# Optimization experiments

Measured on AMD Instinct MI355X. Metric: run time of the kernel, lower is better.

Reference implementation:

```python
import jax, jax.numpy as jnp
import numpy as np

NUM_HEADS = 6

def setup_inputs() -> dict:
    key = jax.random.key(0)
    k1, k2, k3, k4 = jax.random.split(key, 4)
    B, T, C = 128, 256, 384
    s = 1.0 / np.sqrt(C)
    return {
        'x': jax.random.normal(k1, (B, T, C), dtype=jnp.float32),
        'Wq': jax.random.normal(k2, (C, C), dtype=jnp.float32) * s,
        'Wk': jax.random.normal(k3, (C, C), dtype=jnp.float32) * s,
        'Wv': jax.random.normal(k4, (C, C), dtype=jnp.float32) * s,
    }

def reference(x, Wq, Wk, Wv):
    B, T, C = x.shape
    H = NUM_HEADS
    d = C // H
    # projections (bias-free Linear), split into heads
    q = (x @ Wq).reshape(B, T, H, d)
    k = (x @ Wk).reshape(B, T, H, d)
    v = (x @ Wv).reshape(B, T, H, d)
    # NOTE: original scales by 1/sqrt(C), not 1/sqrt(head_dim)
    scale = 1.0 / jnp.sqrt(jnp.asarray(C, dtype=x.dtype))
    att = jnp.einsum('bqhd,bkhd->bhqk', q, k) * scale  # [B,H,T,T]
    causal = jnp.tril(jnp.ones((T, T), dtype=bool))
    att = jnp.where(causal, att, -jnp.inf)
    att = jax.nn.softmax(att, axis=-1)
    # dropout is identity in eval/deterministic mode
    out = jnp.einsum('bhqk,bkhd->bqhd', att, v)  # [B,T,H,d]
    return out.reshape(B, T, C)
```

## Files before the change

kernel.cpp:

```cpp
#include <hip/hip_runtime.h>


typedef unsigned short u16;
typedef float f32x4 __attribute__((ext_vector_type(4)));
typedef short s16x8 __attribute__((ext_vector_type(8)));
typedef u16 u16x4 __attribute__((ext_vector_type(4)));

static constexpr int BB = 128;
static constexpr int TT = 256;
static constexpr int CC = 384;
static constexpr int HH = 6;
static constexpr int DD = 64;
static constexpr int MM = BB * TT;

static constexpr size_t WTOFF = 0;
static constexpr size_t XOFF  = (size_t)3 * CC * CC;

static constexpr float CSC = 0.07362242194579907f;

__device__ __forceinline__ u16 f2bf(float f) {
  unsigned u = __float_as_uint(f);
  u += 0x7fffu + ((u >> 16) & 1u);
  return (u16)(u >> 16);
}

__device__ __forceinline__ void g2l16(const u16* g, u16* l) {
  __builtin_amdgcn_global_load_lds(
      (const __attribute__((address_space(1))) u16*)g,
      (__attribute__((address_space(3))) u16*)l, 16, 0, 0);
}

__global__ void prep(const float* __restrict__ X, const float* __restrict__ Wq,
                     const float* __restrict__ Wk, const float* __restrict__ Wv,
                     u16* __restrict__ ws) {
  int bx = blockIdx.x;
  if (bx < 6144) {
    size_t i = (size_t)(bx * 256 + threadIdx.x) * 8;
    f32x4 a0 = *(const f32x4*)(X + i);
    f32x4 a1 = *(const f32x4*)(X + i + 4);
    s16x8 ab;
#pragma unroll
    for (int j = 0; j < 4; ++j) { ab[j] = (short)f2bf(a0[j]); ab[4 + j] = (short)f2bf(a1[j]); }
    *(s16x8*)(ws + XOFF + i) = ab;
  } else {
    __shared__ u16 Lt[64][66];
    int j = bx - 6144;
    int z = j / 36, t = j % 36, ti = t / 6, tj = t % 6;
    const float* W = (z == 0) ? Wq : (z == 1) ? Wk : Wv;
    const float sc = (z == 0) ? CSC : 1.0f;
    u16* WT = ws + WTOFF + (size_t)z * CC * CC;
    const int rl = threadIdx.x >> 4;
    const int cl = (threadIdx.x & 15) * 4;
#pragma unroll
    for (int it = 0; it < 4; ++it) {
      int r = it * 16 + rl;
      f32x4 v = *(const f32x4*)(W + (size_t)(ti * 64 + r) * CC + tj * 64 + cl);
#pragma unroll
      for (int q = 0; q < 4; ++q) Lt[r][cl + q] = f2bf(v[q] * sc);
    }
    __syncthreads();
#pragma unroll
    for (int it = 0; it < 4; ++it) {
      int n = it * 16 + rl;
      u16x4 o;
#pragma unroll
      for (int q = 0; q < 4; ++q) o[q] = Lt[cl + q][n];
      *(u16x4*)(WT + (size_t)(tj * 64 + n) * CC + ti * 64 + cl) = o;
    }
  }
}

__global__ __launch_bounds__(512, 2) void fused(const u16* __restrict__ ws,
                                                float* __restrict__ out) {
  const int bid = blockIdx.x;
  const int xc = bid & 7;
  const int g5 = bid >> 3;
  const int b = xc * 16 + g5 / 6;
  const int h = g5 % 6;

  __shared__ u16 R1[256][64];
  __shared__ u16 R2[16384];
  __shared__ u16 Ks[256][64];
  __shared__ u16 VTs[64][256];

  const int tid = threadIdx.x;
  const int lane = tid & 63;
  const int w = tid >> 6;
  const int quad = lane >> 4;
  const int col = lane & 15;

  const u16* Xg = ws + XOFF + (size_t)b * TT * CC;
  const u16* Wg = ws + WTOFF;
  u16* Wst = R2;

  const int rl = lane >> 3;
  const int gb = (lane & 7) ^ rl;

  const int wm = (w >> 1) * 64;
  const int wn = (w & 1) * 96;

  auto stage = [&](int kt) {
#pragma unroll
    for (int i = 0; i < 4; ++i) {
      int r0 = w * 32 + i * 8;
      g2l16(Xg + (size_t)(r0 + rl) * CC + kt * 64 + gb * 8, &R1[r0][0]);
    }
#pragma unroll
    for (int i = 0; i < 3; ++i) {
      int r0 = w * 24 + i * 8;
      int rr = r0 + rl;
      int z = rr >> 6, nn = rr & 63;
      g2l16(Wg + (size_t)(z * CC + h * DD + nn) * CC + kt * 64 + gb * 8,
            Wst + r0 * 64);
    }
  };

  f32x4 acc[4][6] = {};

  stage(0);
  __syncthreads();

  for (int kt = 0; kt < 6; ++kt) {
    s16x8 af[4][2], bf[6][2];
#pragma unroll
    for (int mt = 0; mt < 4; ++mt)
#pragma unroll
      for (int ks = 0; ks < 2; ++ks)
        af[mt][ks] = *(const s16x8*)(&R1[wm + mt * 16 + col]
                                        [(((ks * 4 + quad) ^ (col & 7)) * 8)]);
#pragma unroll
    for (int nt = 0; nt < 6; ++nt)
#pragma unroll
      for (int ks = 0; ks < 2; ++ks)
        bf[nt][ks] = *(const s16x8*)(Wst + (wn + nt * 16 + col) * 64 +
                                     (((ks * 4 + quad) ^ (col & 7)) * 8));

    __syncthreads();
    if (kt < 5) stage(kt + 1);

    __builtin_amdgcn_s_setprio(1);
#pragma unroll
    for (int ks = 0; ks < 2; ++ks)
#pragma unroll
      for (int mt = 0; mt < 4; ++mt)
#pragma unroll
        for (int nt = 0; nt < 6; ++nt)
          acc[mt][nt] = __builtin_amdgcn_mfma_f32_16x16x32_bf16(
              af[mt][ks], bf[nt][ks], acc[mt][nt], 0, 0, 0);
    __builtin_amdgcn_s_setprio(0);

    if (kt < 5) __syncthreads();
  }

#pragma unroll
  for (int mt = 0; mt < 4; ++mt) {
    int tokb = wm + mt * 16 + quad * 4;
#pragma unroll
    for (int nt = 0; nt < 6; ++nt) {
      int gn = wn + nt * 16 + col;
      if (gn < 128) {
        u16* dst = (gn < 64) ? &R1[0][0] : &Ks[0][0];
        int d = gn & 63;
#pragma unroll
        for (int r = 0; r < 4; ++r) {
          int tok = tokb + r;
          dst[tok * 64 + (d ^ ((tok & 7) << 3))] = f2bf(acc[mt][nt][r]);
        }
      } else {
        int d = gn - 128;
        uint2 pk;
        pk.x = (unsigned)f2bf(acc[mt][nt][0]) | ((unsigned)f2bf(acc[mt][nt][1]) << 16);
        pk.y = (unsigned)f2bf(acc[mt][nt][2]) | ((unsigned)f2bf(acc[mt][nt][3]) << 16);
        *(uint2*)((u16*)VTs + d * 256 + (tokb ^ ((d & 15) << 3))) = pk;
      }
    }
  }
  __syncthreads();

  const int g0 = w, g1 = 15 - w;
  const int k0max = g0 >> 2, k1max = g1 >> 2;
  const int qq0 = (g0 & 3) * 16 + col;
  const int qq1 = (g1 & 3) * 16 + col;
  u16* PsA = R2 + w * 2048;
  u16* PsB = PsA + 1024;

  s16x8 qf[2][2];
  {
    int qr0 = g0 * 16 + col, qr1 = g1 * 16 + col;
#pragma unroll
    for (int ks = 0; ks < 2; ++ks) {
      qf[0][ks] = *(const s16x8*)(&R1[qr0][(((ks * 4 + quad) ^ (col & 7)) * 8)]);
      qf[1][ks] = *(const s16x8*)(&R1[qr1][(((ks * 4 + quad) ^ (col & 7)) * 8)]);
    }
  }

  f32x4 o[2][4] = {};
  float mst[2] = {-1.0e30f, -1.0e30f}, lst[2] = {0.0f, 0.0f};

  auto sm = [&](f32x4 (&s)[4], bool diag, int qq, float& m, float& l,
                unsigned (&pk)[4][2]) -> float {
    float rmax = -1.0e30f;
#pragma unroll
    for (int nt = 0; nt < 4; ++nt)
#pragma unroll
      for (int r = 0; r < 4; ++r) {
        float t = s[nt][r];
        if (diag && (nt * 16 + quad * 4 + r) > qq) t = -1.0e30f;
        s[nt][r] = t;
        rmax = fmaxf(rmax, t);
      }
    rmax = fmaxf(rmax, __shfl_xor(rmax, 16));
    rmax = fmaxf(rmax, __shfl_xor(rmax, 32));
    float mn = fmaxf(m, rmax);
    float alpha = exp2f(m - mn);
    m = mn;
    float lsum = 0.0f;
#pragma unroll
    for (int nt = 0; nt < 4; ++nt) {
      float p0 = exp2f(s[nt][0] - mn), p1 = exp2f(s[nt][1] - mn);
      float p2 = exp2f(s[nt][2] - mn), p3 = exp2f(s[nt][3] - mn);
      lsum += (p0 + p1) + (p2 + p3);
      pk[nt][0] = (unsigned)f2bf(p0) | ((unsigned)f2bf(p1) << 16);
      pk[nt][1] = (unsigned)f2bf(p2) | ((unsigned)f2bf(p3) << 16);
    }
    l = l * alpha + lsum;
    return alpha;
  };

  for (int kt = 0; kt <= k1max; ++kt) {
    const bool both = (kt <= k0max);

    s16x8 kf[4][2], vf[4][2];
#pragma unroll
    for (int nt = 0; nt < 4; ++nt)
#pragma unroll
      for (int ks = 0; ks < 2; ++ks) {
        int key = kt * 64 + nt * 16 + col;
        kf[nt][ks] = *(const s16x8*)(&Ks[key][(((ks * 4 + quad) ^ (col & 7)) * 8)]);
        int d = nt * 16 + col;
        vf[nt][ks] = *(const s16x8*)((const u16*)VTs + d * 256 +
                     ((kt * 64 + ks * 32 + quad * 8) ^ ((d & 15) << 3)));
      }

    f32x4 sA[4] = {}, sB[4] = {};
    __builtin_amdgcn_s_setprio(1);
    if (both) {
#pragma unroll
      for (int ks = 0; ks < 2; ++ks)
#pragma unroll
        for (int nt = 0; nt < 4; ++nt)
          sA[nt] = __builtin_amdgcn_mfma_f32_16x16x32_bf16(kf[nt][ks], qf[0][ks],
                                                           sA[nt], 0, 0, 0);
    }
#pragma unroll
    for (int ks = 0; ks < 2; ++ks)
#pragma unroll
      for (int nt = 0; nt < 4; ++nt)
        sB[nt] = __builtin_amdgcn_mfma_f32_16x16x32_bf16(kf[nt][ks], qf[1][ks],
                                                         sB[nt], 0, 0, 0);
    __builtin_amdgcn_s_setprio(0);

    unsigned pkA[4][2], pkB[4][2];
    float aA = 1.0f, aB;
    if (both) {
      aA = sm(sA, kt == k0max, qq0, mst[0], lst[0], pkA);
#pragma unroll
      for (int nt = 0; nt < 4; ++nt)
        *(uint2*)(PsA + col * 64 + ((nt * 16 + quad * 4) ^ ((col & 7) << 3))) =
            make_uint2(pkA[nt][0], pkA[nt][1]);
    }
    aB = sm(sB, kt == k1max, qq1, mst[1], lst[1], pkB);
#pragma unroll
    for (int nt = 0; nt < 4; ++nt)
      *(uint2*)(PsB + col * 64 + ((nt * 16 + quad * 4) ^ ((col & 7) << 3))) =
          make_uint2(pkB[nt][0], pkB[nt][1]);

    if (both) {
#pragma unroll
      for (int dt = 0; dt < 4; ++dt)
#pragma unroll
        for (int r = 0; r < 4; ++r) o[0][dt][r] *= aA;
    }
#pragma unroll
    for (int dt = 0; dt < 4; ++dt)
#pragma unroll
      for (int r = 0; r < 4; ++r) o[1][dt][r] *= aB;

    asm volatile("s_waitcnt lgkmcnt(0)" ::: "memory");

    s16x8 pfA[2], pfB[2];
    if (both) {
#pragma unroll
      for (int ks = 0; ks < 2; ++ks)
        pfA[ks] = *(const s16x8*)(PsA + col * 64 +
                                  ((ks * 32 + quad * 8) ^ ((col & 7) << 3)));
    }
#pragma unroll
    for (int ks = 0; ks < 2; ++ks)
      pfB[ks] = *(const s16x8*)(PsB + col * 64 +
                                ((ks * 32 + quad * 8) ^ ((col & 7) << 3)));

    __builtin_amdgcn_s_setprio(1);
    if (both) {
#pragma unroll
      for (int ks = 0; ks < 2; ++ks)
#pragma unroll
        for (int dt = 0; dt < 4; ++dt)
          o[0][dt] = __builtin_amdgcn_mfma_f32_16x16x32_bf16(vf[dt][ks], pfA[ks],
                                                             o[0][dt], 0, 0, 0);
    }
#pragma unroll
    for (int ks = 0; ks < 2; ++ks)
#pragma unroll
      for (int dt = 0; dt < 4; ++dt)
        o[1][dt] = __builtin_amdgcn_mfma_f32_16x16x32_bf16(vf[dt][ks], pfB[ks],
                                                           o[1][dt], 0, 0, 0);
    __builtin_amdgcn_s_setprio(0);
  }

#pragma unroll
  for (int gi = 0; gi < 2; ++gi) {
    int g = gi ? g1 : g0;
    float l = lst[gi];
    l += __shfl_xor(l, 16);
    l += __shfl_xor(l, 32);
    float inv = 1.0f / l;
    int q = g * 16 + col;
#pragma unroll
    for (int dt = 0; dt < 4; ++dt) {
      f32x4 res;
#pragma unroll
      for (int r = 0; r < 4; ++r) res[r] = o[gi][dt][r] * inv;
      *(f32x4*)(out + (size_t)(b * TT + q) * CC + h * DD + dt * 16 + quad * 4) = res;
    }
  }
}

extern "C" void kernel_launch(void* const* d_in, const int* in_sizes, int n_in,
                              void* d_out, int out_size, void* d_ws, size_t ws_size,
                              hipStream_t stream) {
  const float* x  = (const float*)d_in[0];
  const float* wq = (const float*)d_in[1];
  const float* wk = (const float*)d_in[2];
  const float* wv = (const float*)d_in[3];
  u16* ws  = (u16*)d_ws;
  float* out = (float*)d_out;

  prep<<<dim3(6144 + 108), 256, 0, stream>>>(x, wq, wk, wv, ws);
  fused<<<dim3(BB * HH), 512, 0, stream>>>(ws, out);
}
```

Baseline: 154.9 us.

## Double-buffer projection staging, use packed bf16 convert, defer softmax rescale

The QKV projection loop now uses two X and W LDS buffers and prefetches two k-steps ahead. It waits with explicit vmcnt counts and a barrier instead of two __syncthreads per step, aiming to overlap global-to-LDS loads with MFMA work. Float-to-bf16 conversion switches from manual rounding to the hardware v_cvt_pk_bf16_f32 instruction. The online softmax skips the running-max update and output rescale when the new max exceeds the old one by at most 8 across the wave, trading a bounded growth of un-normalised values for fewer exp and multiply ops. The reuse of LDS regions changes: Q and K now live in the X buffers and P in the W buffers.

```diff
diff --git a/kernel.cpp b/kernel.cpp
--- a/kernel.cpp
+++ b/kernel.cpp
@@ -22,6 +22,12 @@
   unsigned u = __float_as_uint(f);
   u += 0x7fffu + ((u >> 16) & 1u);
   return (u16)(u >> 16);
+}
+
+__device__ __forceinline__ unsigned cvtpk(float lo, float hi) {
+  unsigned r;
+  asm("v_cvt_pk_bf16_f32 %0, %1, %2" : "=v"(r) : "v"(lo), "v"(hi));
+  return r;
 }
 
 __device__ __forceinline__ void g2l16(const u16* g, u16* l) {
@@ -78,9 +84,8 @@
   const int b = xc * 16 + g5 / 6;
   const int h = g5 % 6;
 
-  __shared__ u16 R1[256][64];
-  __shared__ u16 R2[16384];
-  __shared__ u16 Ks[256][64];
+  __shared__ u16 X2[2][256][64];
+  __shared__ u16 W2[2][192][64];
   __shared__ u16 VTs[64][256];
 
   const int tid = threadIdx.x;
@@ -91,7 +96,6 @@
 
   const u16* Xg = ws + XOFF + (size_t)b * TT * CC;
   const u16* Wg = ws + WTOFF;
-  u16* Wst = R2;
 
   const int rl = lane >> 3;
   const int gb = (lane & 7) ^ rl;
@@ -100,10 +104,11 @@
   const int wn = (w & 1) * 96;
 
   auto stage = [&](int kt) {
+    int bufi = kt & 1;
 #pragma unroll
     for (int i = 0; i < 4; ++i) {
       int r0 = w * 32 + i * 8;
-      g2l16(Xg + (size_t)(r0 + rl) * CC + kt * 64 + gb * 8, &R1[r0][0]);
+      g2l16(Xg + (size_t)(r0 + rl) * CC + kt * 64 + gb * 8, &X2[bufi][r0][0]);
     }
 #pragma unroll
     for (int i = 0; i < 3; ++i) {
@@ -111,32 +116,42 @@
       int rr = r0 + rl;
       int z = rr >> 6, nn = rr & 63;
       g2l16(Wg + (size_t)(z * CC + h * DD + nn) * CC + kt * 64 + gb * 8,
-            Wst + r0 * 64);
+            &W2[bufi][r0][0]);
     }
   };
 
   f32x4 acc[4][6] = {};
 
   stage(0);
-  __syncthreads();
+  stage(1);
 
   for (int kt = 0; kt < 6; ++kt) {
+    if (kt < 5) asm volatile("s_waitcnt vmcnt(7)" ::: "memory");
+    else        asm volatile("s_waitcnt vmcnt(0)" ::: "memory");
+    __builtin_amdgcn_s_barrier();
+    __builtin_amdgcn_sched_barrier(0);
+
+    const int bufi = kt & 1;
     s16x8 af[4][2], bf[6][2];
 #pragma unroll
     for (int mt = 0; mt < 4; ++mt)
 #pragma unroll
       for (int ks = 0; ks < 2; ++ks)
-        af[mt][ks] = *(const s16x8*)(&R1[wm + mt * 16 + col]
+        af[mt][ks] = *(const s16x8*)(&X2[bufi][wm + mt * 16 + col]
                                         [(((ks * 4 + quad) ^ (col & 7)) * 8)]);
 #pragma unroll
     for (int nt = 0; nt < 6; ++nt)
 #pragma unroll
       for (int ks = 0; ks < 2; ++ks)
-        bf[nt][ks] = *(const s16x8*)(Wst + (wn + nt * 16 + col) * 64 +
-                                     (((ks * 4 + quad) ^ (col & 7)) * 8));
-
-    __syncthreads();
-    if (kt < 5) stage(kt + 1);
+        bf[nt][ks] = *(const s16x8*)(&W2[bufi][wn + nt * 16 + col]
+                                        [(((ks * 4 + quad) ^ (col & 7)) * 8)]);
+
+    if (kt < 4) {
+      asm volatile("s_waitcnt lgkmcnt(0)" ::: "memory");
+      __builtin_amdgcn_s_barrier();
+      __builtin_amdgcn_sched_barrier(0);
+      stage(kt + 2);
+    }
 
     __builtin_amdgcn_s_setprio(1);
 #pragma unroll
@@ -148,30 +163,31 @@
           acc[mt][nt] = __builtin_amdgcn_mfma_f32_16x16x32_bf16(
               af[mt][ks], bf[nt][ks], acc[mt][nt], 0, 0, 0);
     __builtin_amdgcn_s_setprio(0);
-
-    if (kt < 5) __syncthreads();
-  }
-
+  }
+
+  __syncthreads();
+
+  u16* Qb  = &X2[0][0][0];
+  u16* KsB = &X2[1][0][0];
 #pragma unroll
   for (int mt = 0; mt < 4; ++mt) {
     int tokb = wm + mt * 16 + quad * 4;
 #pragma unroll
     for (int nt = 0; nt < 6; ++nt) {
       int gn = wn + nt * 16 + col;
+      unsigned u01 = cvtpk(acc[mt][nt][0], acc[mt][nt][1]);
+      unsigned u23 = cvtpk(acc[mt][nt][2], acc[mt][nt][3]);
       if (gn < 128) {
-        u16* dst = (gn < 64) ? &R1[0][0] : &Ks[0][0];
+        u16* dst = (gn < 64) ? Qb : KsB;
         int d = gn & 63;
-#pragma unroll
-        for (int r = 0; r < 4; ++r) {
-          int tok = tokb + r;
-          dst[tok * 64 + (d ^ ((tok & 7) << 3))] = f2bf(acc[mt][nt][r]);
-        }
+        dst[(tokb + 0) * 64 + (d ^ (((tokb + 0) & 7) << 3))] = (u16)u01;
+        dst[(tokb + 1) * 64 + (d ^ (((tokb + 1) & 7) << 3))] = (u16)(u01 >> 16);
+        dst[(tokb + 2) * 64 + (d ^ (((tokb + 2) & 7) << 3))] = (u16)u23;
+        dst[(tokb + 3) * 64 + (d ^ (((tokb + 3) & 7) << 3))] = (u16)(u23 >> 16);
       } else {
         int d = gn - 128;
-        uint2 pk;
-        pk.x = (unsigned)f2bf(acc[mt][nt][0]) | ((unsigned)f2bf(acc[mt][nt][1]) << 16);
-        pk.y = (unsigned)f2bf(acc[mt][nt][2]) | ((unsigned)f2bf(acc[mt][nt][3]) << 16);
-        *(uint2*)((u16*)VTs + d * 256 + (tokb ^ ((d & 15) << 3))) = pk;
+        *(uint2*)((u16*)VTs + d * 256 + (tokb ^ ((d & 15) << 3))) =
+            make_uint2(u01, u23);
       }
     }
   }
@@ -181,7 +197,7 @@
   const int k0max = g0 >> 2, k1max = g1 >> 2;
   const int qq0 = (g0 & 3) * 16 + col;
   const int qq1 = (g1 & 3) * 16 + col;
-  u16* PsA = R2 + w * 2048;
+  u16* PsA = (u16*)W2 + w * 2048;
   u16* PsB = PsA + 1024;
 
   s16x8 qf[2][2];
@@ -189,8 +205,8 @@
     int qr0 = g0 * 16 + col, qr1 = g1 * 16 + col;
 #pragma unroll
     for (int ks = 0; ks < 2; ++ks) {
-      qf[0][ks] = *(const s16x8*)(&R1[qr0][(((ks * 4 + quad) ^ (col & 7)) * 8)]);
-      qf[1][ks] = *(const s16x8*)(&R1[qr1][(((ks * 4 + quad) ^ (col & 7)) * 8)]);
+      qf[0][ks] = *(const s16x8*)(Qb + qr0 * 64 + (((ks * 4 + quad) ^ (col & 7)) * 8));
+      qf[1][ks] = *(const s16x8*)(Qb + qr1 * 64 + (((ks * 4 + quad) ^ (col & 7)) * 8));
     }
   }
 
@@ -198,30 +214,36 @@
   float mst[2] = {-1.0e30f, -1.0e30f}, lst[2] = {0.0f, 0.0f};
 
   auto sm = [&](f32x4 (&s)[4], bool diag, int qq, float& m, float& l,
-                unsigned (&pk)[4][2]) -> float {
-    float rmax = -1.0e30f;
-#pragma unroll
-    for (int nt = 0; nt < 4; ++nt)
-#pragma unroll
-      for (int r = 0; r < 4; ++r) {
-        float t = s[nt][r];
-        if (diag && (nt * 16 + quad * 4 + r) > qq) t = -1.0e30f;
-        s[nt][r] = t;
-        rmax = fmaxf(rmax, t);
+                unsigned (&pk)[4][2], bool& deferred) -> float {
+    float mx[4];
+#pragma unroll
+    for (int nt = 0; nt < 4; ++nt) {
+      if (diag) {
+#pragma unroll
+        for (int r = 0; r < 4; ++r)
+          if ((nt * 16 + quad * 4 + r) > qq) s[nt][r] = -1.0e30f;
       }
+      mx[nt] = fmaxf(fmaxf(s[nt][0], s[nt][1]), fmaxf(s[nt][2], s[nt][3]));
+    }
+    float rmax = fmaxf(fmaxf(mx[0], mx[1]), fmaxf(mx[2], mx[3]));
     rmax = fmaxf(rmax, __shfl_xor(rmax, 16));
     rmax = fmaxf(rmax, __shfl_xor(rmax, 32));
-    float mn = fmaxf(m, rmax);
-    float alpha = exp2f(m - mn);
-    m = mn;
+
+    deferred = __all(rmax - m <= 8.0f);
+    float alpha = 1.0f;
+    if (!deferred) {
+      float mn = fmaxf(m, rmax);
+      alpha = exp2f(m - mn);
+      m = mn;
+    }
     float lsum = 0.0f;
 #pragma unroll
     for (int nt = 0; nt < 4; ++nt) {
-      float p0 = exp2f(s[nt][0] - mn), p1 = exp2f(s[nt][1] - mn);
-      float p2 = exp2f(s[nt][2] - mn), p3 = exp2f(s[nt][3] - mn);
+      float p0 = exp2f(s[nt][0] - m), p1 = exp2f(s[nt][1] - m);
+      float p2 = exp2f(s[nt][2] - m), p3 = exp2f(s[nt][3] - m);
       lsum += (p0 + p1) + (p2 + p3);
-      pk[nt][0] = (unsigned)f2bf(p0) | ((unsigned)f2bf(p1) << 16);
-      pk[nt][1] = (unsigned)f2bf(p2) | ((unsigned)f2bf(p3) << 16);
+      pk[nt][0] = cvtpk(p0, p1);
+      pk[nt][1] = cvtpk(p2, p3);
     }
     l = l * alpha + lsum;
     return alpha;
@@ -236,7 +258,8 @@
 #pragma unroll
       for (int ks = 0; ks < 2; ++ks) {
         int key = kt * 64 + nt * 16 + col;
-        kf[nt][ks] = *(const s16x8*)(&Ks[key][(((ks * 4 + quad) ^ (col & 7)) * 8)]);
+        kf[nt][ks] = *(const s16x8*)(KsB + key * 64 +
+                                     (((ks * 4 + quad) ^ (col & 7)) * 8));
         int d = nt * 16 + col;
         vf[nt][ks] = *(const s16x8*)((const u16*)VTs + d * 256 +
                      ((kt * 64 + ks * 32 + quad * 8) ^ ((d & 15) << 3)));
@@ -261,30 +284,33 @@
     __builtin_amdgcn_s_setprio(0);
 
     unsigned pkA[4][2], pkB[4][2];
+    bool dfA = true, dfB;
     float aA = 1.0f, aB;
     if (both) {
-      aA = sm(sA, kt == k0max, qq0, mst[0], lst[0], pkA);
+      aA = sm(sA, kt == k0max, qq0, mst[0], lst[0], pkA, dfA);
 #pragma unroll
       for (int nt = 0; nt < 4; ++nt)
         *(uint2*)(PsA + col * 64 + ((nt * 16 + quad * 4) ^ ((col & 7) << 3))) =
             make_uint2(pkA[nt][0], pkA[nt][1]);
     }
-    aB = sm(sB, kt == k1max, qq1, mst[1], lst[1], pkB);
+    aB = sm(sB, kt == k1max, qq1, mst[1], lst[1], pkB, dfB);
 #pragma unroll
     for (int nt = 0; nt < 4; ++nt)
       *(uint2*)(PsB + col * 64 + ((nt * 16 + quad * 4) ^ ((col & 7) << 3))) =
           make_uint2(pkB[nt][0], pkB[nt][1]);
 
-    if (both) {
+    if (both && !dfA) {
 #pragma unroll
       for (int dt = 0; dt < 4; ++dt)
 #pragma unroll
         for (int r = 0; r < 4; ++r) o[0][dt][r] *= aA;
     }
-#pragma unroll
-    for (int dt = 0; dt < 4; ++dt)
-#pragma unroll
-      for (int r = 0; r < 4; ++r) o[1][dt][r] *= aB;
+    if (!dfB) {
+#pragma unroll
+      for (int dt = 0; dt < 4; ++dt)
+#pragma unroll
+        for (int r = 0; r < 4; ++r) o[1][dt][r] *= aB;
+    }
 
     asm volatile("s_waitcnt lgkmcnt(0)" ::: "memory");
 
```

New measurement: 151.2 us. 1.02x faster.
